# Performance work log

Hardware: AMD Instinct MI355X
Metric: run time of the kernel (lower is better)

## Reference

```python
import jax, jax.numpy as jnp
import numpy as np

B, C, F, J = 64, 16, 2048, 25
EMBED, CLASSES, NJ = 64, 5, 12
AFFECT = slice(0, 12)
UNAFFECT = slice(12, 24)


def setup_inputs() -> dict:
    key = jax.random.key(0)
    k0, k1, k2, k3 = jax.random.split(key, 4)
    features = jax.random.normal(k0, (B, C, F, J), dtype=jnp.float32)
    W1 = jax.random.normal(k1, (EMBED, C, NJ), dtype=jnp.float32) * 0.05
    b1 = jnp.zeros((EMBED,), jnp.float32)
    W2 = jax.random.normal(k2, (EMBED, C, NJ), dtype=jnp.float32) * 0.05
    b2 = jnp.zeros((EMBED,), jnp.float32)
    Wl = jax.random.normal(k3, (CLASSES, 16 * EMBED), dtype=jnp.float32) * 0.02
    bl = jnp.zeros((CLASSES,), jnp.float32)
    return {"features": features, "W1": W1, "b1": b1, "W2": W2, "b2": b2, "Wl": Wl, "bl": bl}


def _stat_features(x, proto):
    # x: [b, c, f, j]; single sort shared by min/max/quantiles/median
    f = x.shape[-2]
    xs = jnp.sort(x, axis=-2)

    def quant(p):
        # torch.quantile linear interpolation
        pos = p * (f - 1)
        lo = int(np.floor(pos)); hi = int(np.ceil(pos)); frac = np.float32(pos - lo)
        return xs[..., lo, :] * (1.0 - frac) + xs[..., hi, :] * frac

    s1 = xs[..., 0, :]                       # min
    s2 = xs[..., -1, :]                      # max
    s3 = quant(0.25)
    s4 = xs[..., (f - 1) // 2, :]            # torch.median: lower middle element
    s5 = quant(0.75)
    s6 = jnp.mean(x, axis=-2)
    s7 = jnp.std(x, axis=-2, ddof=1)         # torch.std unbiased
    s8 = s2 - s1
    z = (x - s6[..., None, :]) / s7[..., None, :]
    if proto:
        s9 = jnp.mean(z ** 3, axis=-2)       # skew
    else:
        s9 = jnp.mean(z ** 4, axis=-2) - 3.0  # excess kurtosis
    return jnp.stack([s2, s3, s4, s5, s6, s7, s8, s9], axis=-2)  # [b, c, 8, j]


def _fuse(stat, W, b):
    # Conv2d kernel (1, joints) == contraction over (c, j) per stat row
    out = jnp.einsum('bcsj,ecj->bes', stat, W) + b[None, :, None]
    return out.reshape(out.shape[0], -1)  # flatten (embed, stats) like torch.flatten


def reference(features, W1, b1, W2, b2, Wl, bl):
    affected = features[:, :, :, AFFECT]
    unaffected = features[:, :, :, UNAFFECT]
    stat_af = _stat_features(affected, proto=False)
    stat_ua = _stat_features(unaffected, proto=False)
    # attn=False path (STAT_VA block disabled)
    stat1 = _stat_features(unaffected + affected, proto=True)
    _ = _fuse(stat1, W1, b1)  # stat1 branch only feeds CL loss (get_cl_loss=False)
    stat2 = jnp.concatenate([stat_af, stat_ua], axis=-2)  # [b, c, 16, j]
    flat2 = _fuse(stat2, W2, b2)                          # [b, 16*embed]
    logits = flat2 @ Wl.T + bl
    return logits
```

## Files before the change

kernel.cpp:

```cpp
#include <hip/hip_runtime.h>
#include <hip/hip_bf16.h>
#include <math.h>


#define F_LEN 2048
#define JTOT 25
#define STATS_PER_BC 192
#define LP 2056

typedef float f4a __attribute__((ext_vector_type(4), aligned(4)));

__device__ __forceinline__ int swz(int i) {
  return (i & ~31) | ((i + ((i >> 5) << 2)) & 31);
}

template <int PAT>
__device__ __forceinline__ float ds_swz(float v) {
  return __int_as_float(
      __builtin_amdgcn_ds_swizzle(__float_as_int(v), PAT));
}

template <int CTRL, int BANK>
__device__ __forceinline__ int upd_dpp(int old_, int src) {
  return __builtin_amdgcn_update_dpp(old_, src, CTRL, 0xF, BANK, false);
}

__device__ __forceinline__ float xpartner(float v, const int lm,
                                          const int addr32) {
  const int vi = __float_as_int(v);
  switch (lm) {
    case 1:
      return __int_as_float(upd_dpp<0xB1, 0xF>(vi, vi));
    case 2:
      return __int_as_float(upd_dpp<0x4E, 0xF>(vi, vi));
    case 4: {
      const int t1 = upd_dpp<0x104, 0x5>(vi, vi);
      const int t2 = upd_dpp<0x114, 0xA>(t1, vi);
      return __int_as_float(t2);
    }
    case 8:
      return __int_as_float(upd_dpp<0x128, 0xF>(vi, vi));
    case 16:
      return ds_swz<0x401F>(v);
    default:
      return __int_as_float(
          __builtin_amdgcn_ds_bpermute(addr32, vi));
  }
}

__device__ __forceinline__ float wave_sum(float v, int addr32) {
  v += xpartner(v, 1, addr32);
  v += xpartner(v, 2, addr32);
  v += xpartner(v, 4, addr32);
  v += xpartner(v, 8, addr32);
  v += xpartner(v, 16, addr32);
  v += xpartner(v, 32, addr32);
  return v;
}

__device__ __forceinline__ void read_x(const float* wlds, int lane,
                                       float* x) {
  const float4* src4 = (const float4*)wlds;
#pragma unroll
  for (int q = 0; q < 8; ++q) {
    float4 v = src4[lane * 8 + ((lane + q) & 7)];
    x[4 * q] = v.x;
    x[4 * q + 1] = v.y;
    x[4 * q + 2] = v.z;
    x[4 * q + 3] = v.w;
  }
}

__device__ __forceinline__ void merge7(const float* wlds, int lane,
                                       float& val, float& mn, float& mx) {
  const int kk = (lane == 0) ? 511
               : (lane == 1) ? 512
               : (lane == 2) ? 1023
               : (lane == 3) ? 1535 : 1536;
  const int mtot = kk + 1;
  int lo = mtot - 1024; if (lo < 0) lo = 0;
  int hi = (mtot < 1024) ? mtot : 1024;
  for (int it = 0; it < 11; ++it) {
    const bool act = lo < hi;
    const int s = (lo + hi) >> 1;
    const int sa = (s < 1023) ? s : 1023;
    float Av = wlds[swz(sa)];
    Av = (s < 1024) ? Av : INFINITY;
    int bidx = mtot - s - 1;
    bidx = bidx < 0 ? 0 : (bidx > 1023 ? 1023 : bidx);
    const float Bv = wlds[swz(2047 - bidx)];
    const bool gg = act && (Bv > Av);
    if (gg) lo = s + 1;
    else if (act) hi = s;
  }
  {
    const int s = lo;
    const int ia = (s - 1 < 0) ? 0 : s - 1;
    const float fa = wlds[swz(ia)];
    const float fromA = (s > 0) ? fa : -INFINITY;
    const int bi = mtot - s - 1;
    const int ib = (bi < 0) ? 0 : bi;
    const float fb = wlds[swz(2047 - ib)];
    const float fromB = (bi >= 0) ? fb : -INFINITY;
    val = fmaxf(fromA, fromB);
  }
  if (lane == 0) {
    mn = fminf(wlds[swz(0)], wlds[swz(2047)]);
    mx = fmaxf(wlds[swz(1023)], wlds[swz(1024)]);
  }
}

__global__ __launch_bounds__(256, 4) void stat_kernel(
    const float* __restrict__ Fp, float* __restrict__ stat2) {
  __shared__ float lds[2 * LP];
  const int g = blockIdx.x;
  const int xcd = g & 7;
  const int mm = g >> 3;
  const int bc = xcd * 128 + mm / 6;
  const int grp = mm % 6;
  const int t = threadIdx.x;
  const int w = t >> 6;
  const int lane = t & 63;
  const int addr32 = ((lane ^ 32) << 2);
  const int j0 = grp * 4;

  float vz[8], vw[8];
  const int rot = (t + ((t >> 5) << 2)) & 31;
  float* p0 = lds + (t & ~31) + rot;
  {
    const float* bbase = Fp + (size_t)bc * F_LEN * JTOT + j0;
#pragma unroll
    for (int it = 0; it < 8; ++it) {
      const int f = it * 256 + t;
      f4a v = *reinterpret_cast<const f4a*>(bbase + (size_t)f * JTOT);
      p0[it * 256] = v.x;
      p0[LP + it * 256] = v.y;
      vz[it] = v.z;
      vw[it] = v.w;
    }
  }
  __syncthreads();

  float x[32];
  if (w < 2) read_x(lds + w * LP, lane, x);
  __syncthreads();

  {
#pragma unroll
    for (int it = 0; it < 8; ++it) {
      p0[it * 256] = vz[it];
      p0[LP + it * 256] = vw[it];
    }
  }
  __syncthreads();
  if (w >= 2) read_x(lds + (w - 2) * LP, lane, x);

  float sum = 0.f;
#pragma unroll
  for (int e = 0; e < 32; ++e) sum += x[e];
  sum = wave_sum(sum, addr32);
  const float m = sum * (1.0f / 2048.0f);

  float c2 = 0.f, c4 = 0.f;
#pragma unroll
  for (int e = 0; e < 32; ++e) {
    float d = x[e] - m;
    float dd = d * d;
    c2 += dd;
    c4 += dd * dd;
  }
  c2 = wave_sum(c2, addr32);
  c4 = wave_sum(c4, addr32);
  const float var = c2 * (1.0f / 2047.0f);
  const float sd = sqrtf(var);
  const float kurt = (c4 * (1.0f / 2048.0f)) / (var * var) - 3.0f;

#pragma unroll
  for (int kp = 1; kp <= 4; ++kp) {
    const int k = 1 << kp;
#pragma unroll
    for (int jp = kp - 1; jp >= 0; --jp) {
      const int st = 1 << jp;
#pragma unroll
      for (int e = 0; e < 32; ++e) {
        if ((e & st) == 0) {
          const bool up = ((e & k) == 0);
          float a = x[e], b = x[e + st];
          float lo2 = fminf(a, b), hi2 = fmaxf(a, b);
          x[e] = up ? lo2 : hi2;
          x[e + st] = up ? hi2 : lo2;
        }
      }
    }
  }

  unsigned Fst = 0u;
#pragma unroll
  for (int kp = 5; kp <= 10; ++kp) {
    const unsigned d = ((lane >> (kp - 5)) & 1) ? 0x80000000u : 0u;
#pragma unroll
    for (int jp = kp - 1; jp >= 5; --jp) {
      const int lm = 1 << (jp - 5);
      const unsigned r = ((lane >> (jp - 5)) & 1) ? 0x80000000u : 0u;
      const unsigned tgt = d ^ r;
      const unsigned fl = tgt ^ Fst;
      Fst = tgt;
      float o[32];
#pragma unroll
      for (int e = 0; e < 32; ++e)
        x[e] = __uint_as_float(__float_as_uint(x[e]) ^ fl);
#pragma unroll
      for (int e = 0; e < 32; ++e) o[e] = xpartner(x[e], lm, addr32);
#pragma unroll
      for (int e = 0; e < 32; ++e)
        x[e] = fminf(x[e], -o[e]);
    }
    {
      const unsigned fl = d ^ Fst;
      Fst = d;
#pragma unroll
      for (int e = 0; e < 32; ++e)
        x[e] = __uint_as_float(__float_as_uint(x[e]) ^ fl);
    }
#pragma unroll
    for (int jp = 4; jp >= 0; --jp) {
      const int st = 1 << jp;
#pragma unroll
      for (int e = 0; e < 32; ++e) {
        if ((e & st) == 0) {
          float a = x[e], b = x[e + st];
          x[e] = fminf(a, b);
          x[e + st] = fmaxf(a, b);
        }
      }
    }
  }
#pragma unroll
  for (int e = 0; e < 32; ++e)
    x[e] = __uint_as_float(__float_as_uint(x[e]) ^ Fst);

  float* wl2 = lds + (w & 1) * LP;
  float val = 0.f, mn = 0.f, mx = 0.f;
  if (w < 2) {
    float4* dst4 = (float4*)wl2;
#pragma unroll
    for (int q = 0; q < 8; ++q) {
      int wq = 8 * lane + ((q + lane) & 7);
      dst4[wq] = make_float4(x[4 * q], x[4 * q + 1], x[4 * q + 2], x[4 * q + 3]);
    }
  }
  __syncthreads();
  if (w < 2) merge7(wl2, lane, val, mn, mx);
  __syncthreads();
  if (w >= 2) {
    float4* dst4 = (float4*)wl2;
#pragma unroll
    for (int q = 0; q < 8; ++q) {
      int wq = 8 * lane + ((q + lane) & 7);
      dst4[wq] = make_float4(x[4 * q], x[4 * q + 1], x[4 * q + 2], x[4 * q + 3]);
    }
  }
  __syncthreads();
  if (w >= 2) merge7(wl2, lane, val, mn, mx);

  const float a511 = __shfl(val, 0, 64);
  const float a512 = __shfl(val, 1, 64);
  const float amed = __shfl(val, 2, 64);
  const float a1535 = __shfl(val, 3, 64);
  const float a1536 = __shfl(val, 4, 64);

  if (lane == 0) {
    const float q25 = 0.25f * a511 + 0.75f * a512;
    const float q75 = 0.75f * a1535 + 0.25f * a1536;
    const int j = j0 + w;
    const int jj = (j < 12) ? j : j - 12;
    const int sb = (j < 12) ? 0 : 8;
    float st8[8] = {mx, q25, amed, q75, m, sd, mx - mn, kurt};
    float* o = stat2 + (bc * 16 + sb) * 12 + jj;
#pragma unroll
    for (int s2 = 0; s2 < 8; ++s2) o[s2 * 12] = st8[s2];
  }
}

__global__ __launch_bounds__(256) void prep_kernel(
    const float* __restrict__ W2, const float* __restrict__ b2,
    const float* __restrict__ Wl, const float* __restrict__ bl,
    float* __restrict__ M, float* __restrict__ C) {
  const int g = blockIdx.x;
  const int t = threadIdx.x;
  if (g < 60) {
    const int id = g * 256 + t;
    const int k = id / 3072;
    const int r = id % 3072;
    const int c = r / 192;
    const int s = (r % 192) / 12;
    const int j = r % 12;
    const float* wl = Wl + k * 1024 + s;
    const float* w2 = W2 + c * 12 + j;
    float acc = 0.f;
#pragma unroll 8
    for (int e = 0; e < 64; ++e) acc += wl[e * 16] * w2[e * 192];
    M[id] = acc;
  } else if (t < 64) {
    const int e = t;
    const int addr32 = ((e ^ 32) << 2);
    for (int k = 0; k < 5; ++k) {
      const float* wl = Wl + k * 1024 + e * 16;
      float rs = 0.f;
#pragma unroll
      for (int s = 0; s < 16; ++s) rs += wl[s];
      float v = wave_sum(rs * b2[e], addr32);
      if (e == 0) C[k] = v + bl[k];
    }
  }
}

__global__ __launch_bounds__(256) void logits_kernel(
    const float* __restrict__ stat2, const float* __restrict__ M,
    const float* __restrict__ C, float* __restrict__ out) {
  __shared__ float s_red[20];
  const int b = blockIdx.x;
  const int t = threadIdx.x;
  const int lane = t & 63;
  const int w = t >> 6;
  const int addr32 = ((lane ^ 32) << 2);

  float acc[5] = {0.f, 0.f, 0.f, 0.f, 0.f};
#pragma unroll
  for (int ii = 0; ii < 12; ++ii) {
    const int i = ii * 256 + t;
    const float s = stat2[b * 3072 + i];
#pragma unroll
    for (int k = 0; k < 5; ++k) acc[k] += s * M[k * 3072 + i];
  }
#pragma unroll
  for (int k = 0; k < 5; ++k) acc[k] = wave_sum(acc[k], addr32);
  if (lane == 0) {
#pragma unroll
    for (int k = 0; k < 5; ++k) s_red[w * 5 + k] = acc[k];
  }
  __syncthreads();
  if (t < 5)
    out[b * 5 + t] =
        s_red[t] + s_red[5 + t] + s_red[10 + t] + s_red[15 + t] + C[t];
}

extern "C" void kernel_launch(void* const* d_in, const int* in_sizes, int n_in,
                              void* d_out, int out_size, void* d_ws,
                              size_t ws_size, hipStream_t stream) {
  const float* Fp = (const float*)d_in[0];
  const float* W2 = (const float*)d_in[3];
  const float* b2 = (const float*)d_in[4];
  const float* Wl = (const float*)d_in[5];
  const float* bl = (const float*)d_in[6];
  float* out = (float*)d_out;

  float* stat2 = (float*)d_ws;
  float* M = stat2 + 196608;
  float* C = M + 15360;

  prep_kernel<<<61, 256, 0, stream>>>(W2, b2, Wl, bl, M, C);
  stat_kernel<<<6144, 256, 0, stream>>>(Fp, stat2);
  logits_kernel<<<64, 256, 0, stream>>>(stat2, M, C, out);
}
```

Baseline: 449.3 us.

## Process two joint columns per wave to halve blocks and interleave sorts

Each block now loads 8 joint columns instead of 4 and each wave sorts and reduces two columns (x and y) together, with interleaved cross-lane exchanges and paired wave reductions. Grid size is halved, LDS per block doubles, and launch bounds drop to 2 blocks per CU. The aim is more instruction-level parallelism to hide the latency of the DPP/swizzle shuffles, plus fewer barriers because each wave now has its own LDS region for the merge step. The cost is roughly double the register pressure (two 32-element arrays plus staging buffers) and lower occupancy, which could cause spills or less latency hiding.

```diff
diff --git a/kernel.cpp b/kernel.cpp
--- a/kernel.cpp
+++ b/kernel.cpp
@@ -58,6 +58,16 @@
   return v;
 }
 
+__device__ __forceinline__ void wave_sum2(float& a, float& b, int addr32) {
+#pragma unroll
+  for (int lm = 1; lm <= 32; lm <<= 1) {
+    float pa = xpartner(a, lm, addr32);
+    float pb = xpartner(b, lm, addr32);
+    a += pa;
+    b += pb;
+  }
+}
+
 __device__ __forceinline__ void read_x(const float* wlds, int lane,
                                        float* x) {
   const float4* src4 = (const float4*)wlds;
@@ -68,6 +78,17 @@
     x[4 * q + 1] = v.y;
     x[4 * q + 2] = v.z;
     x[4 * q + 3] = v.w;
+  }
+}
+
+__device__ __forceinline__ void dump_x(float* wlds, int lane,
+                                       const float* x) {
+  float4* dst4 = (float4*)wlds;
+#pragma unroll
+  for (int q = 0; q < 8; ++q) {
+    int wq = 8 * lane + ((q + lane) & 7);
+    dst4[wq] =
+        make_float4(x[4 * q], x[4 * q + 1], x[4 * q + 2], x[4 * q + 3]);
   }
 }
 
@@ -110,21 +131,23 @@
   }
 }
 
-__global__ __launch_bounds__(256, 4) void stat_kernel(
+__global__ __launch_bounds__(256, 2) void stat_kernel(
     const float* __restrict__ Fp, float* __restrict__ stat2) {
-  __shared__ float lds[2 * LP];
+  __shared__ float lds[4 * LP];
   const int g = blockIdx.x;
   const int xcd = g & 7;
   const int mm = g >> 3;
-  const int bc = xcd * 128 + mm / 6;
-  const int grp = mm % 6;
+  const int bc = xcd * 128 + mm / 3;
+  const int grp = mm % 3;
   const int t = threadIdx.x;
   const int w = t >> 6;
   const int lane = t & 63;
   const int addr32 = ((lane ^ 32) << 2);
-  const int j0 = grp * 4;
-
-  float vz[8], vw[8];
+  const int j0 = grp * 8;
+  const int cx = j0 + ((w < 2) ? w : w + 2);
+  const int cy = cx + 2;
+
+  float az[8], aw[8], bz[8], bw[8];
   const int rot = (t + ((t >> 5) << 2)) & 31;
   float* p0 = lds + (t & ~31) + rot;
   {
@@ -132,48 +155,57 @@
 #pragma unroll
     for (int it = 0; it < 8; ++it) {
       const int f = it * 256 + t;
-      f4a v = *reinterpret_cast<const f4a*>(bbase + (size_t)f * JTOT);
-      p0[it * 256] = v.x;
-      p0[LP + it * 256] = v.y;
-      vz[it] = v.z;
-      vw[it] = v.w;
+      f4a va = *reinterpret_cast<const f4a*>(bbase + (size_t)f * JTOT);
+      f4a vb = *reinterpret_cast<const f4a*>(bbase + (size_t)f * JTOT + 4);
+      p0[it * 256] = va.x;
+      p0[LP + it * 256] = va.y;
+      p0[2 * LP + it * 256] = vb.x;
+      p0[3 * LP + it * 256] = vb.y;
+      az[it] = va.z; aw[it] = va.w;
+      bz[it] = vb.z; bw[it] = vb.w;
     }
   }
   __syncthreads();
 
-  float x[32];
-  if (w < 2) read_x(lds + w * LP, lane, x);
+  float x[32], y[32];
+  read_x(lds + w * LP, lane, x);
   __syncthreads();
 
   {
 #pragma unroll
     for (int it = 0; it < 8; ++it) {
-      p0[it * 256] = vz[it];
-      p0[LP + it * 256] = vw[it];
+      p0[it * 256] = az[it];
+      p0[LP + it * 256] = aw[it];
+      p0[2 * LP + it * 256] = bz[it];
+      p0[3 * LP + it * 256] = bw[it];
     }
   }
   __syncthreads();
-  if (w >= 2) read_x(lds + (w - 2) * LP, lane, x);
-
-  float sum = 0.f;
-#pragma unroll
-  for (int e = 0; e < 32; ++e) sum += x[e];
-  sum = wave_sum(sum, addr32);
-  const float m = sum * (1.0f / 2048.0f);
-
-  float c2 = 0.f, c4 = 0.f;
+  read_x(lds + w * LP, lane, y);
+
+  float sx = 0.f, sy = 0.f;
+#pragma unroll
+  for (int e = 0; e < 32; ++e) { sx += x[e]; sy += y[e]; }
+  wave_sum2(sx, sy, addr32);
+  const float mx_m = sx * (1.0f / 2048.0f);
+  const float my_m = sy * (1.0f / 2048.0f);
+
+  float c2x = 0.f, c4x = 0.f, c2y = 0.f, c4y = 0.f;
 #pragma unroll
   for (int e = 0; e < 32; ++e) {
-    float d = x[e] - m;
-    float dd = d * d;
-    c2 += dd;
-    c4 += dd * dd;
-  }
-  c2 = wave_sum(c2, addr32);
-  c4 = wave_sum(c4, addr32);
-  const float var = c2 * (1.0f / 2047.0f);
-  const float sd = sqrtf(var);
-  const float kurt = (c4 * (1.0f / 2048.0f)) / (var * var) - 3.0f;
+    float dx = x[e] - mx_m, dy = y[e] - my_m;
+    float ddx = dx * dx, ddy = dy * dy;
+    c2x += ddx; c4x += ddx * ddx;
+    c2y += ddy; c4y += ddy * ddy;
+  }
+  wave_sum2(c2x, c2y, addr32);
+  wave_sum2(c4x, c4y, addr32);
+  const float varx = c2x * (1.0f / 2047.0f);
+  const float vary = c2y * (1.0f / 2047.0f);
+  const float sdx = sqrtf(varx);
+  const float sdy = sqrtf(vary);
+  const float kurtx = (c4x * (1.0f / 2048.0f)) / (varx * varx) - 3.0f;
+  const float kurty = (c4y * (1.0f / 2048.0f)) / (vary * vary) - 3.0f;
 
 #pragma unroll
   for (int kp = 1; kp <= 4; ++kp) {
@@ -185,10 +217,18 @@
       for (int e = 0; e < 32; ++e) {
         if ((e & st) == 0) {
           const bool up = ((e & k) == 0);
-          float a = x[e], b = x[e + st];
-          float lo2 = fminf(a, b), hi2 = fmaxf(a, b);
-          x[e] = up ? lo2 : hi2;
-          x[e + st] = up ? hi2 : lo2;
+          {
+            float a = x[e], b = x[e + st];
+            float lo2 = fminf(a, b), hi2 = fmaxf(a, b);
+            x[e] = up ? lo2 : hi2;
+            x[e + st] = up ? hi2 : lo2;
+          }
+          {
+            float a = y[e], b = y[e + st];
+            float lo2 = fminf(a, b), hi2 = fmaxf(a, b);
+            y[e] = up ? lo2 : hi2;
+            y[e + st] = up ? hi2 : lo2;
+          }
         }
       }
     }
@@ -205,22 +245,27 @@
       const unsigned tgt = d ^ r;
       const unsigned fl = tgt ^ Fst;
       Fst = tgt;
-      float o[32];
-#pragma unroll
-      for (int e = 0; e < 32; ++e)
+#pragma unroll
+      for (int e = 0; e < 32; ++e) {
         x[e] = __uint_as_float(__float_as_uint(x[e]) ^ fl);
-#pragma unroll
-      for (int e = 0; e < 32; ++e) o[e] = xpartner(x[e], lm, addr32);
-#pragma unroll
-      for (int e = 0; e < 32; ++e)
-        x[e] = fminf(x[e], -o[e]);
+        y[e] = __uint_as_float(__float_as_uint(y[e]) ^ fl);
+      }
+#pragma unroll
+      for (int e = 0; e < 32; ++e) {
+        float ox = xpartner(x[e], lm, addr32);
+        float oy = xpartner(y[e], lm, addr32);
+        x[e] = fminf(x[e], -ox);
+        y[e] = fminf(y[e], -oy);
+      }
     }
     {
       const unsigned fl = d ^ Fst;
       Fst = d;
 #pragma unroll
-      for (int e = 0; e < 32; ++e)
+      for (int e = 0; e < 32; ++e) {
         x[e] = __uint_as_float(__float_as_uint(x[e]) ^ fl);
+        y[e] = __uint_as_float(__float_as_uint(y[e]) ^ fl);
+      }
     }
 #pragma unroll
     for (int jp = 4; jp >= 0; --jp) {
@@ -228,57 +273,66 @@
 #pragma unroll
       for (int e = 0; e < 32; ++e) {
         if ((e & st) == 0) {
-          float a = x[e], b = x[e + st];
-          x[e] = fminf(a, b);
-          x[e + st] = fmaxf(a, b);
+          {
+            float a = x[e], b = x[e + st];
+            x[e] = fminf(a, b);
+            x[e + st] = fmaxf(a, b);
+          }
+          {
+            float a = y[e], b = y[e + st];
+            y[e] = fminf(a, b);
+            y[e + st] = fmaxf(a, b);
+          }
         }
       }
     }
   }
 #pragma unroll
-  for (int e = 0; e < 32; ++e)
+  for (int e = 0; e < 32; ++e) {
     x[e] = __uint_as_float(__float_as_uint(x[e]) ^ Fst);
-
-  float* wl2 = lds + (w & 1) * LP;
-  float val = 0.f, mn = 0.f, mx = 0.f;
-  if (w < 2) {
-    float4* dst4 = (float4*)wl2;
-#pragma unroll
-    for (int q = 0; q < 8; ++q) {
-      int wq = 8 * lane + ((q + lane) & 7);
-      dst4[wq] = make_float4(x[4 * q], x[4 * q + 1], x[4 * q + 2], x[4 * q + 3]);
-    }
-  }
-  __syncthreads();
-  if (w < 2) merge7(wl2, lane, val, mn, mx);
-  __syncthreads();
-  if (w >= 2) {
-    float4* dst4 = (float4*)wl2;
-#pragma unroll
-    for (int q = 0; q < 8; ++q) {
-      int wq = 8 * lane + ((q + lane) & 7);
-      dst4[wq] = make_float4(x[4 * q], x[4 * q + 1], x[4 * q + 2], x[4 * q + 3]);
-    }
-  }
-  __syncthreads();
-  if (w >= 2) merge7(wl2, lane, val, mn, mx);
-
-  const float a511 = __shfl(val, 0, 64);
-  const float a512 = __shfl(val, 1, 64);
-  const float amed = __shfl(val, 2, 64);
-  const float a1535 = __shfl(val, 3, 64);
-  const float a1536 = __shfl(val, 4, 64);
+    y[e] = __uint_as_float(__float_as_uint(y[e]) ^ Fst);
+  }
+
+  float* wreg = lds + w * LP;
+  float valx = 0.f, mnx = 0.f, mxx = 0.f;
+  float valy = 0.f, mny = 0.f, mxy = 0.f;
+  dump_x(wreg, lane, x);
+  merge7(wreg, lane, valx, mnx, mxx);
+  dump_x(wreg, lane, y);
+  merge7(wreg, lane, valy, mny, mxy);
+
+  const float a511x = __shfl(valx, 0, 64);
+  const float a512x = __shfl(valx, 1, 64);
+  const float amedx = __shfl(valx, 2, 64);
+  const float a1535x = __shfl(valx, 3, 64);
+  const float a1536x = __shfl(valx, 4, 64);
+  const float a511y = __shfl(valy, 0, 64);
+  const float a512y = __shfl(valy, 1, 64);
+  const float amedy = __shfl(valy, 2, 64);
+  const float a1535y = __shfl(valy, 3, 64);
+  const float a1536y = __shfl(valy, 4, 64);
 
   if (lane == 0) {
-    const float q25 = 0.25f * a511 + 0.75f * a512;
-    const float q75 = 0.75f * a1535 + 0.25f * a1536;
-    const int j = j0 + w;
-    const int jj = (j < 12) ? j : j - 12;
-    const int sb = (j < 12) ? 0 : 8;
-    float st8[8] = {mx, q25, amed, q75, m, sd, mx - mn, kurt};
-    float* o = stat2 + (bc * 16 + sb) * 12 + jj;
-#pragma unroll
-    for (int s2 = 0; s2 < 8; ++s2) o[s2 * 12] = st8[s2];
+    {
+      const float q25 = 0.25f * a511x + 0.75f * a512x;
+      const float q75 = 0.75f * a1535x + 0.25f * a1536x;
+      const int jj = (cx < 12) ? cx : cx - 12;
+      const int sb = (cx < 12) ? 0 : 8;
+      float st8[8] = {mxx, q25, amedx, q75, mx_m, sdx, mxx - mnx, kurtx};
+      float* o = stat2 + (bc * 16 + sb) * 12 + jj;
+#pragma unroll
+      for (int s2 = 0; s2 < 8; ++s2) o[s2 * 12] = st8[s2];
+    }
+    {
+      const float q25 = 0.25f * a511y + 0.75f * a512y;
+      const float q75 = 0.75f * a1535y + 0.25f * a1536y;
+      const int jj = (cy < 12) ? cy : cy - 12;
+      const int sb = (cy < 12) ? 0 : 8;
+      float st8[8] = {mxy, q25, amedy, q75, my_m, sdy, mxy - mny, kurty};
+      float* o = stat2 + (bc * 16 + sb) * 12 + jj;
+#pragma unroll
+      for (int s2 = 0; s2 < 8; ++s2) o[s2 * 12] = st8[s2];
+    }
   }
 }
 
@@ -360,6 +414,6 @@
   float* C = M + 15360;
 
   prep_kernel<<<61, 256, 0, stream>>>(W2, b2, Wl, bl, M, C);
-  stat_kernel<<<6144, 256, 0, stream>>>(Fp, stat2);
+  stat_kernel<<<3072, 256, 0, stream>>>(Fp, stat2);
   logits_kernel<<<64, 256, 0, stream>>>(stat2, M, C, out);
 }
```

Result: faster. 430.9 us (-4.1%).

## Give each wave its own LDS slab and drop staged two-phase sort loads

Applied to the files above, without the earlier changes.

The stat kernel now allocates four LDS slabs, one per wave, instead of two shared slabs that waves took turns using. Loads become scalar, strided per joint, and written straight into a swizzled layout, which removes the extra barriers and serialised phases around the sort and merge. The partner-exchange loop is fused so no 32-element temporary array is kept, and the in-register merge stages are trimmed in early rounds. In exchange, LDS use per block doubles, which may lower occupancy now that the min-blocks launch bound was removed, and the global loads are narrower and may coalesce less well.

```diff
diff --git a/kernel.cpp b/kernel.cpp
--- a/kernel.cpp
+++ b/kernel.cpp
@@ -7,8 +7,6 @@
 #define JTOT 25
 #define STATS_PER_BC 192
 #define LP 2056
-
-typedef float f4a __attribute__((ext_vector_type(4), aligned(4)));
 
 __device__ __forceinline__ int swz(int i) {
   return (i & ~31) | ((i + ((i >> 5) << 2)) & 31);
@@ -58,21 +56,136 @@
   return v;
 }
 
-__device__ __forceinline__ void read_x(const float* wlds, int lane,
-                                       float* x) {
-  const float4* src4 = (const float4*)wlds;
-#pragma unroll
-  for (int q = 0; q < 8; ++q) {
-    float4 v = src4[lane * 8 + ((lane + q) & 7)];
-    x[4 * q] = v.x;
-    x[4 * q + 1] = v.y;
-    x[4 * q + 2] = v.z;
-    x[4 * q + 3] = v.w;
-  }
-}
-
-__device__ __forceinline__ void merge7(const float* wlds, int lane,
-                                       float& val, float& mn, float& mx) {
+__global__ __launch_bounds__(256) void stat_kernel(
+    const float* __restrict__ Fp, float* __restrict__ stat2) {
+  __shared__ float lds[4 * LP];
+  const int g = blockIdx.x;
+  const int xcd = g & 7;
+  const int mm = g >> 3;
+  const int bc = xcd * 128 + mm / 6;
+  const int grp = mm % 6;
+  const int t = threadIdx.x;
+  const int w = t >> 6;
+  const int lane = t & 63;
+  const int addr32 = ((lane ^ 32) << 2);
+  const int j0 = grp * 4;
+  float* wlds = lds + w * LP;
+
+  {
+    const float* bbase = Fp + (size_t)bc * F_LEN * JTOT + j0;
+    const int f0 = t >> 2, jj = t & 3;
+    float* ldst = lds + jj * LP;
+#pragma unroll
+    for (int it = 0; it < 32; ++it) {
+      const int f = it * 64 + f0;
+      ldst[swz(f)] = bbase[(size_t)f * JTOT + jj];
+    }
+  }
+  __syncthreads();
+
+  float x[32];
+  {
+    const float4* src4 = (const float4*)wlds;
+#pragma unroll
+    for (int q = 0; q < 8; ++q) {
+      float4 v = src4[lane * 8 + ((lane + q) & 7)];
+      x[4 * q] = v.x; x[4 * q + 1] = v.y;
+      x[4 * q + 2] = v.z; x[4 * q + 3] = v.w;
+    }
+  }
+
+  float sum = 0.f;
+#pragma unroll
+  for (int e = 0; e < 32; ++e) sum += x[e];
+  sum = wave_sum(sum, addr32);
+  const float m = sum * (1.0f / 2048.0f);
+
+  float c2 = 0.f, c4 = 0.f;
+#pragma unroll
+  for (int e = 0; e < 32; ++e) {
+    float d = x[e] - m;
+    float dd = d * d;
+    c2 += dd;
+    c4 += dd * dd;
+  }
+  c2 = wave_sum(c2, addr32);
+  c4 = wave_sum(c4, addr32);
+  const float var = c2 * (1.0f / 2047.0f);
+  const float sd = sqrtf(var);
+  const float kurt = (c4 * (1.0f / 2048.0f)) / (var * var) - 3.0f;
+
+#pragma unroll
+  for (int kp = 1; kp <= 4; ++kp) {
+    const int k = 1 << kp;
+#pragma unroll
+    for (int jp = kp - 1; jp >= 0; --jp) {
+      const int st = 1 << jp;
+#pragma unroll
+      for (int e = 0; e < 32; ++e) {
+        if ((e & st) == 0) {
+          const bool up = ((e & k) == 0);
+          float a = x[e], b = x[e + st];
+          float lo2 = fminf(a, b), hi2 = fmaxf(a, b);
+          x[e] = up ? lo2 : hi2;
+          x[e + st] = up ? hi2 : lo2;
+        }
+      }
+    }
+  }
+
+  unsigned Fst = 0u;
+#pragma unroll
+  for (int kp = 5; kp <= 10; ++kp) {
+    const unsigned d = ((lane >> (kp - 5)) & 1) ? 0x80000000u : 0u;
+#pragma unroll
+    for (int jp = kp - 1; jp >= 5; --jp) {
+      const int lm = 1 << (jp - 5);
+      const unsigned r = ((lane >> (jp - 5)) & 1) ? 0x80000000u : 0u;
+      const unsigned tgt = d ^ r;
+      const unsigned fl = tgt ^ Fst;
+      Fst = tgt;
+#pragma unroll
+      for (int e = 0; e < 32; ++e)
+        x[e] = __uint_as_float(__float_as_uint(x[e]) ^ fl);
+#pragma unroll
+      for (int e = 0; e < 32; ++e) {
+        float o = xpartner(x[e], lm, addr32);
+        x[e] = fminf(x[e], -o);
+      }
+    }
+    {
+      const unsigned fl = d ^ Fst;
+      Fst = d;
+#pragma unroll
+      for (int e = 0; e < 32; ++e)
+        x[e] = __uint_as_float(__float_as_uint(x[e]) ^ fl);
+    }
+#pragma unroll
+    for (int jp = (kp - 1 < 4 ? kp - 1 : 4); jp >= 0; --jp) {
+      const int st = 1 << jp;
+#pragma unroll
+      for (int e = 0; e < 32; ++e) {
+        if ((e & st) == 0) {
+          float a = x[e], b = x[e + st];
+          x[e] = fminf(a, b);
+          x[e + st] = fmaxf(a, b);
+        }
+      }
+    }
+  }
+#pragma unroll
+  for (int e = 0; e < 32; ++e)
+    x[e] = __uint_as_float(__float_as_uint(x[e]) ^ Fst);
+
+  {
+    float4* dst4 = (float4*)wlds;
+#pragma unroll
+    for (int q = 0; q < 8; ++q) {
+      int wq = 8 * lane + ((q + lane) & 7);
+      dst4[wq] = make_float4(x[4 * q], x[4 * q + 1], x[4 * q + 2], x[4 * q + 3]);
+    }
+  }
+
   const int kk = (lane == 0) ? 511
                : (lane == 1) ? 512
                : (lane == 2) ? 1023
@@ -93,6 +206,7 @@
     if (gg) lo = s + 1;
     else if (act) hi = s;
   }
+  float val;
   {
     const int s = lo;
     const int ia = (s - 1 < 0) ? 0 : s - 1;
@@ -104,172 +218,16 @@
     const float fromB = (bi >= 0) ? fb : -INFINITY;
     val = fmaxf(fromA, fromB);
   }
-  if (lane == 0) {
-    mn = fminf(wlds[swz(0)], wlds[swz(2047)]);
-    mx = fmaxf(wlds[swz(1023)], wlds[swz(1024)]);
-  }
-}
-
-__global__ __launch_bounds__(256, 4) void stat_kernel(
-    const float* __restrict__ Fp, float* __restrict__ stat2) {
-  __shared__ float lds[2 * LP];
-  const int g = blockIdx.x;
-  const int xcd = g & 7;
-  const int mm = g >> 3;
-  const int bc = xcd * 128 + mm / 6;
-  const int grp = mm % 6;
-  const int t = threadIdx.x;
-  const int w = t >> 6;
-  const int lane = t & 63;
-  const int addr32 = ((lane ^ 32) << 2);
-  const int j0 = grp * 4;
-
-  float vz[8], vw[8];
-  const int rot = (t + ((t >> 5) << 2)) & 31;
-  float* p0 = lds + (t & ~31) + rot;
-  {
-    const float* bbase = Fp + (size_t)bc * F_LEN * JTOT + j0;
-#pragma unroll
-    for (int it = 0; it < 8; ++it) {
-      const int f = it * 256 + t;
-      f4a v = *reinterpret_cast<const f4a*>(bbase + (size_t)f * JTOT);
-      p0[it * 256] = v.x;
-      p0[LP + it * 256] = v.y;
-      vz[it] = v.z;
-      vw[it] = v.w;
-    }
-  }
-  __syncthreads();
-
-  float x[32];
-  if (w < 2) read_x(lds + w * LP, lane, x);
-  __syncthreads();
-
-  {
-#pragma unroll
-    for (int it = 0; it < 8; ++it) {
-      p0[it * 256] = vz[it];
-      p0[LP + it * 256] = vw[it];
-    }
-  }
-  __syncthreads();
-  if (w >= 2) read_x(lds + (w - 2) * LP, lane, x);
-
-  float sum = 0.f;
-#pragma unroll
-  for (int e = 0; e < 32; ++e) sum += x[e];
-  sum = wave_sum(sum, addr32);
-  const float m = sum * (1.0f / 2048.0f);
-
-  float c2 = 0.f, c4 = 0.f;
-#pragma unroll
-  for (int e = 0; e < 32; ++e) {
-    float d = x[e] - m;
-    float dd = d * d;
-    c2 += dd;
-    c4 += dd * dd;
-  }
-  c2 = wave_sum(c2, addr32);
-  c4 = wave_sum(c4, addr32);
-  const float var = c2 * (1.0f / 2047.0f);
-  const float sd = sqrtf(var);
-  const float kurt = (c4 * (1.0f / 2048.0f)) / (var * var) - 3.0f;
-
-#pragma unroll
-  for (int kp = 1; kp <= 4; ++kp) {
-    const int k = 1 << kp;
-#pragma unroll
-    for (int jp = kp - 1; jp >= 0; --jp) {
-      const int st = 1 << jp;
-#pragma unroll
-      for (int e = 0; e < 32; ++e) {
-        if ((e & st) == 0) {
-          const bool up = ((e & k) == 0);
-          float a = x[e], b = x[e + st];
-          float lo2 = fminf(a, b), hi2 = fmaxf(a, b);
-          x[e] = up ? lo2 : hi2;
-          x[e + st] = up ? hi2 : lo2;
-        }
-      }
-    }
-  }
-
-  unsigned Fst = 0u;
-#pragma unroll
-  for (int kp = 5; kp <= 10; ++kp) {
-    const unsigned d = ((lane >> (kp - 5)) & 1) ? 0x80000000u : 0u;
-#pragma unroll
-    for (int jp = kp - 1; jp >= 5; --jp) {
-      const int lm = 1 << (jp - 5);
-      const unsigned r = ((lane >> (jp - 5)) & 1) ? 0x80000000u : 0u;
-      const unsigned tgt = d ^ r;
-      const unsigned fl = tgt ^ Fst;
-      Fst = tgt;
-      float o[32];
-#pragma unroll
-      for (int e = 0; e < 32; ++e)
-        x[e] = __uint_as_float(__float_as_uint(x[e]) ^ fl);
-#pragma unroll
-      for (int e = 0; e < 32; ++e) o[e] = xpartner(x[e], lm, addr32);
-#pragma unroll
-      for (int e = 0; e < 32; ++e)
-        x[e] = fminf(x[e], -o[e]);
-    }
-    {
-      const unsigned fl = d ^ Fst;
-      Fst = d;
-#pragma unroll
-      for (int e = 0; e < 32; ++e)
-        x[e] = __uint_as_float(__float_as_uint(x[e]) ^ fl);
-    }
-#pragma unroll
-    for (int jp = 4; jp >= 0; --jp) {
-      const int st = 1 << jp;
-#pragma unroll
-      for (int e = 0; e < 32; ++e) {
-        if ((e & st) == 0) {
-          float a = x[e], b = x[e + st];
-          x[e] = fminf(a, b);
-          x[e + st] = fmaxf(a, b);
-        }
-      }
-    }
-  }
-#pragma unroll
-  for (int e = 0; e < 32; ++e)
-    x[e] = __uint_as_float(__float_as_uint(x[e]) ^ Fst);
-
-  float* wl2 = lds + (w & 1) * LP;
-  float val = 0.f, mn = 0.f, mx = 0.f;
-  if (w < 2) {
-    float4* dst4 = (float4*)wl2;
-#pragma unroll
-    for (int q = 0; q < 8; ++q) {
-      int wq = 8 * lane + ((q + lane) & 7);
-      dst4[wq] = make_float4(x[4 * q], x[4 * q + 1], x[4 * q + 2], x[4 * q + 3]);
-    }
-  }
-  __syncthreads();
-  if (w < 2) merge7(wl2, lane, val, mn, mx);
-  __syncthreads();
-  if (w >= 2) {
-    float4* dst4 = (float4*)wl2;
-#pragma unroll
-    for (int q = 0; q < 8; ++q) {
-      int wq = 8 * lane + ((q + lane) & 7);
-      dst4[wq] = make_float4(x[4 * q], x[4 * q + 1], x[4 * q + 2], x[4 * q + 3]);
-    }
-  }
-  __syncthreads();
-  if (w >= 2) merge7(wl2, lane, val, mn, mx);
-
-  const float a511 = __shfl(val, 0, 64);
-  const float a512 = __shfl(val, 1, 64);
-  const float amed = __shfl(val, 2, 64);
+
+  const float a511  = __shfl(val, 0, 64);
+  const float a512  = __shfl(val, 1, 64);
+  const float amed  = __shfl(val, 2, 64);
   const float a1535 = __shfl(val, 3, 64);
   const float a1536 = __shfl(val, 4, 64);
 
   if (lane == 0) {
+    const float mn = fminf(wlds[swz(0)], wlds[swz(2047)]);
+    const float mx = fmaxf(wlds[swz(1023)], wlds[swz(1024)]);
     const float q25 = 0.25f * a511 + 0.75f * a512;
     const float q75 = 0.75f * a1535 + 0.25f * a1536;
     const int j = j0 + w;
```

New measurement: 436.2 us. 2.9% less time.
